# Performance work log

Hardware: AMD Instinct MI355X
Metric: run time of the kernel (lower is better)

Reference implementation:

```python
import jax, jax.numpy as jnp
import numpy as np

B = 65536
H = 32  # LSTM hidden size


def _ln(x, g, b, n_axes):
    # torch LayerNorm over the last n_axes dims, eps=1e-5, biased variance
    axes = tuple(range(x.ndim - n_axes, x.ndim))
    m = jnp.mean(x, axes, keepdims=True)
    v = jnp.var(x, axes, keepdims=True)
    return (x - m) * jax.lax.rsqrt(v + 1e-5) * g + b


def _lstm_layer(xs, Wih, Whh, bih, bhh):
    # xs: [T, B, in] ; gate order i,f,g,o as in torch
    Bn = xs.shape[1]
    h0 = jnp.zeros((Bn, H), xs.dtype)
    c0 = jnp.zeros((Bn, H), xs.dtype)
    bias = bih + bhh
    def step(carry, xt):
        h, c = carry
        gates = xt @ Wih.T + h @ Whh.T + bias
        i, f, g, o = jnp.split(gates, 4, axis=-1)
        c = jax.nn.sigmoid(f) * c + jax.nn.sigmoid(i) * jnp.tanh(g)
        h = jax.nn.sigmoid(o) * jnp.tanh(c)
        return (h, c), h
    _, hs = jax.lax.scan(step, (h0, c0), xs)
    return hs  # [T, B, H]


def _conv(x, W, b, pad_w):
    y = jax.lax.conv_general_dilated(
        x, W, (1, 1), [(0, 0), (pad_w, pad_w)],
        dimension_numbers=('NCHW', 'OIHW', 'NCHW'))
    return y + b[None, :, None, None]


def _forward(x,
             lstm_Wih0, lstm_Whh0, lstm_bih0, lstm_bhh0,
             lstm_Wih1, lstm_Whh1, lstm_bih1, lstm_bhh1,
             lstm_fcW, lstm_fcb,
             cv2_W, cv2_b, cv2_g, cv2_beta,
             cv3_W, cv3_b, cv3_g, cv3_beta,
             f1_W, f1_b, f1_g, f1_beta,
             f2_W, f2_b, f2_g, f2_beta,
             f3_W, f3_b, f3_g, f3_beta):
    Bn = x.shape[0]
    # the nested torch.cat loops are exactly this reshape: [B,12] -> [B,4,3]
    pos = x[:, 0, 1, 104:116].reshape(Bn, 4, 3)
    pos_r = pos[:, 3, :]                       # [B,3]
    # 2-layer LSTM, last-step output -> fc (run under no_grad in original)
    h1 = _lstm_layer(jnp.swapaxes(pos, 0, 1), lstm_Wih0, lstm_Whh0, lstm_bih0, lstm_bhh0)
    h2 = _lstm_layer(h1, lstm_Wih1, lstm_Whh1, lstm_bih1, lstm_bhh1)
    pos_p = h2[-1] @ lstm_fcW.T + lstm_fcb     # [B,3]
    pos_p = jax.lax.stop_gradient(pos_p)       # torch.no_grad in predict()
    vel = (pos_p - pos_r) / 0.1                # [B,3]
    # CSI conv branch
    csi = x[:, :, :, 1:103]                    # [B,1,3,102]
    out2 = jax.nn.relu(_ln(_conv(csi, cv2_W, cv2_b, 2), cv2_g, cv2_beta, 3))   # [B,4,1,102]
    out3 = jax.nn.relu(_ln(_conv(out2, cv3_W, cv3_b, 0), cv3_g, cv3_beta, 3))  # [B,1,1,102]
    out4 = jnp.concatenate([out3[:, 0, 0, :], pos_p, vel], axis=-1)            # [B,108]
    h = jax.nn.relu(_ln(out4 @ f1_W.T + f1_b, f1_g, f1_beta, 1))
    h = jax.nn.relu(_ln(h @ f2_W.T + f2_b, f2_g, f2_beta, 1))
    out = jax.nn.sigmoid(_ln(h @ f3_W.T + f3_b, f3_g, f3_beta, 1))             # [B,102]
    return out


def setup_inputs() -> dict:
    key = jax.random.key(0)
    ks = iter(jax.random.split(key, 64))
    def rn(shape, s=0.05):
        return jax.random.normal(next(ks), shape, jnp.float32) * s
    return dict(
        x=jax.random.normal(next(ks), (B, 1, 3, 116), jnp.float32),
        lstm_Wih0=rn((4 * H, 3)), lstm_Whh0=rn((4 * H, H)),
        lstm_bih0=rn((4 * H,)), lstm_bhh0=rn((4 * H,)),
        lstm_Wih1=rn((4 * H, H)), lstm_Whh1=rn((4 * H, H)),
        lstm_bih1=rn((4 * H,)), lstm_bhh1=rn((4 * H,)),
        lstm_fcW=rn((3, H)), lstm_fcb=rn((3,)),
        cv2_W=rn((4, 1, 3, 5)), cv2_b=rn((4,)),
        cv2_g=jnp.ones((4, 1, 102)), cv2_beta=jnp.zeros((4, 1, 102)),
        cv3_W=rn((1, 4, 1, 1)), cv3_b=rn((1,)),
        cv3_g=jnp.ones((1, 1, 102)), cv3_beta=jnp.zeros((1, 1, 102)),
        f1_W=rn((32, 108)), f1_b=rn((32,)),
        f1_g=jnp.ones((32,)), f1_beta=jnp.zeros((32,)),
        f2_W=rn((32, 32)), f2_b=rn((32,)),
        f2_g=jnp.ones((32,)), f2_beta=jnp.zeros((32,)),
        f3_W=rn((102, 32)), f3_b=rn((102,)),
        f3_g=jnp.ones((102,)), f3_beta=jnp.zeros((102,)),
    )


def reference(x,
              lstm_Wih0, lstm_Whh0, lstm_bih0, lstm_bhh0,
              lstm_Wih1, lstm_Whh1, lstm_bih1, lstm_bhh1,
              lstm_fcW, lstm_fcb,
              cv2_W, cv2_b, cv2_g, cv2_beta,
              cv3_W, cv3_b, cv3_g, cv3_beta,
              f1_W, f1_b, f1_g, f1_beta,
              f2_W, f2_b, f2_g, f2_beta,
              f3_W, f3_b, f3_g, f3_beta):
    return _forward(x,
                    lstm_Wih0, lstm_Whh0, lstm_bih0, lstm_bhh0,
                    lstm_Wih1, lstm_Whh1, lstm_bih1, lstm_bhh1,
                    lstm_fcW, lstm_fcb,
                    cv2_W, cv2_b, cv2_g, cv2_beta,
                    cv3_W, cv3_b, cv3_g, cv3_beta,
                    f1_W, f1_b, f1_g, f1_beta,
                    f2_W, f2_b, f2_g, f2_beta,
                    f3_W, f3_b, f3_g, f3_beta)
```

## Files before the change

kernel.cpp:

```cpp
#include <hip/hip_runtime.h>

#define DI __device__ __forceinline__
#define NSAMP 65536

typedef __attribute__((ext_vector_type(4))) float f32x4;
typedef __attribute__((ext_vector_type(8))) short short8;
typedef __attribute__((ext_vector_type(4))) short short4v;

DI float frcp(float x){ return __builtin_amdgcn_rcpf(x); }
DI float frsq(float x){ return __builtin_amdgcn_rsqf(x); }
DI float sigmf(float x){ return frcp(1.f + __expf(-x)); }
DI float tanhf_(float x){ return 1.f - 2.f*frcp(__expf(2.f*x) + 1.f); }
DI unsigned short f2bf(float f){
  unsigned u = __float_as_uint(f);
  return (unsigned short)((u + 0x7FFFu + ((u>>16)&1u)) >> 16);
}
DI float bf2f(unsigned short h){ return __uint_as_float(((unsigned)h)<<16); }

struct Params {
  const float* __restrict__ x;
  const float* __restrict__ pv;
  const float* __restrict__ ptail;
  const unsigned short* __restrict__ frags;
  const float* __restrict__ Wih0; const float* __restrict__ Whh0;
  const float* __restrict__ bih0; const float* __restrict__ bhh0;
  const float* __restrict__ Wih1; const float* __restrict__ Whh1;
  const float* __restrict__ bih1; const float* __restrict__ bhh1;
  const float* __restrict__ fcW;  const float* __restrict__ fcb;
  const float* __restrict__ W2;   const float* __restrict__ b2;
  const float* __restrict__ g2;   const float* __restrict__ be2;
  const float* __restrict__ W3;   const float* __restrict__ b3;
  const float* __restrict__ g3;   const float* __restrict__ be3;
  const float* __restrict__ W1f;  const float* __restrict__ b1f;
  const float* __restrict__ g1f;  const float* __restrict__ be1f;
  const float* __restrict__ W2f;  const float* __restrict__ b2f;
  const float* __restrict__ g2f;  const float* __restrict__ be2f;
  const float* __restrict__ W3f;  const float* __restrict__ b3f;
  const float* __restrict__ g3f;  const float* __restrict__ be3f;
  float* __restrict__ out;
};

#define PT_G2   0
#define PT_BE2  408
#define PT_G3   816
#define PT_BE3  918
#define PT_B1F  1020
#define PT_G1F  1052
#define PT_BE1F 1084
#define PT_B2F  1116
#define PT_G2F  1148
#define PT_BE2F 1180
#define PT_B3F  1212
#define PT_G3F  1314
#define PT_BE3F 1416
#define PT_N    1518
#define NFRAG   49

__global__ __launch_bounds__(256,1) void prep_kernel(Params p,
    unsigned short* __restrict__ frags, float* __restrict__ bsum,
    float* __restrict__ ptail){
  const int tid = threadIdx.x;
  if(tid < 64){
    const int l15 = tid & 15, g4 = tid >> 4;
    const float* mats[3] = {p.Whh0, p.Wih1, p.Whh1};
    for(int m=0;m<3;m++)
      for(int t=0;t<8;t++){
        const int n = 16*t + l15;
        unsigned short* dst = &frags[((size_t)(m*8+t)*64 + tid)*8];
        for(int j=0;j<4;j++){
          dst[j]   = f2bf(mats[m][n*32 + 4*g4 + j]);
          dst[4+j] = f2bf(mats[m][n*32 + 16 + 4*g4 + j]);
        }
      }
    for(int t=0;t<8;t++){
      const int n = 16*t + l15;
      unsigned short* dst = &frags[((size_t)(24+t)*64 + tid)*8];
      for(int j=0;j<4;j++){
        int k = 4*g4 + j;
        dst[j]   = (k < 3) ? f2bf(p.Wih0[n*3 + k]) : (unsigned short)0;
        dst[4+j] = 0;
      }
    }
    for(int kc=0;kc<4;kc++)
      for(int nt=0;nt<2;nt++){
        const int n = nt*16 + l15;
        unsigned short* dst = &frags[((size_t)(32+kc*2+nt)*64 + tid)*8];
        for(int j=0;j<4;j++){
          int k0 = kc*32 + 4*g4 + j;
          int k1 = kc*32 + 16 + 4*g4 + j;
          dst[j]   = (k0<108) ? f2bf(p.W1f[n*108+k0]) : (unsigned short)0;
          dst[4+j] = (k1<108) ? f2bf(p.W1f[n*108+k1]) : (unsigned short)0;
        }
      }
    for(int nt=0;nt<2;nt++){
      const int n = nt*16 + l15;
      unsigned short* dst = &frags[((size_t)(40+nt)*64 + tid)*8];
      for(int j=0;j<4;j++){
        dst[j]   = f2bf(p.W2f[n*32 + 4*g4 + j]);
        dst[4+j] = f2bf(p.W2f[n*32 + 16 + 4*g4 + j]);
      }
    }
    for(int nt=0;nt<7;nt++){
      const int n2 = nt*16 + l15;
      unsigned short* dst = &frags[((size_t)(42+nt)*64 + tid)*8];
      for(int j=0;j<4;j++){
        int k0 = 4*g4 + j, k1 = 16 + 4*g4 + j;
        dst[j]   = (n2<102) ? f2bf(p.W3f[n2*32+k0]) : (unsigned short)0;
        dst[4+j] = (n2<102) ? f2bf(p.W3f[n2*32+k1]) : (unsigned short)0;
      }
    }
  } else if(tid < 192){
    int i = tid - 64;
    bsum[i]       = p.bih0[i] + p.bhh0[i];
    bsum[128 + i] = p.bih1[i] + p.bhh1[i];
  }
  for(int i=tid;i<408;i+=256){ ptail[PT_G2+i]=p.g2[i]; ptail[PT_BE2+i]=p.be2[i]; }
  for(int i=tid;i<102;i+=256){
    ptail[PT_G3+i]=p.g3[i];   ptail[PT_BE3+i]=p.be3[i];
    ptail[PT_B3F+i]=p.b3f[i]; ptail[PT_G3F+i]=p.g3f[i]; ptail[PT_BE3F+i]=p.be3f[i];
  }
  if(tid<32){
    ptail[PT_B1F+tid]=p.b1f[tid];   ptail[PT_G1F+tid]=p.g1f[tid];
    ptail[PT_BE1F+tid]=p.be1f[tid]; ptail[PT_B2F+tid]=p.b2f[tid];
    ptail[PT_G2F+tid]=p.g2f[tid];   ptail[PT_BE2F+tid]=p.be2f[tid];
  }
}

DI short8 mk_afrag(const float* hbase, int l15, int g4){
  const float4* p0 = (const float4*)(hbase + l15*36 + 4*g4);
  const float4* p1 = (const float4*)(hbase + l15*36 + 16 + 4*g4);
  float4 lo = *p0; float4 hi = *p1;
  short8 s;
  s[0]=(short)f2bf(lo.x); s[1]=(short)f2bf(lo.y); s[2]=(short)f2bf(lo.z); s[3]=(short)f2bf(lo.w);
  s[4]=(short)f2bf(hi.x); s[5]=(short)f2bf(hi.y); s[6]=(short)f2bf(hi.z); s[7]=(short)f2bf(hi.w);
  return s;
}
DI short8 mk_af16(const unsigned short* lb, int off){
  short4v lo = *(const short4v*)(lb + off);
  short4v hi = *(const short4v*)(lb + off + 16);
  short8 s;
  s[0]=lo[0]; s[1]=lo[1]; s[2]=lo[2]; s[3]=lo[3];
  s[4]=hi[0]; s[5]=hi[1]; s[6]=hi[2]; s[7]=hi[3];
  return s;
}
DI short8 mk_af16_lo(const unsigned short* lb, int off){
  short4v lo = *(const short4v*)(lb + off);
  short8 s;
  s[0]=lo[0]; s[1]=lo[1]; s[2]=lo[2]; s[3]=lo[3];
  s[4]=0; s[5]=0; s[6]=0; s[7]=0;
  return s;
}

__global__ __launch_bounds__(256,1) void lstm_kernel(
    const float* __restrict__ x, const unsigned short* __restrict__ frags,
    const float* __restrict__ bsum, const float* __restrict__ fcW,
    const float* __restrict__ fcb, float* __restrict__ pv){
  __shared__ float hb[4][2][16][36];
  const int tid = threadIdx.x;
  const int w = tid >> 6, l = tid & 63;
  const int l15 = l & 15, g4 = l >> 4;
  const int base = blockIdx.x*64 + w*16;
  const float* __restrict__ xrow = x + (size_t)(base + l15)*348;

  short8 wf[4][8];
  const short8* fsrc = (const short8*)frags;
  #pragma unroll
  for(int m=0;m<4;m++)
    #pragma unroll
    for(int t=0;t<8;t++) wf[m][t] = fsrc[(m*8+t)*64 + l];

  float bfr[2][8];
  #pragma unroll
  for(int t=0;t<8;t++){
    bfr[0][t] = bsum[16*t + l15];
    bfr[1][t] = bsum[128 + 16*t + l15];
  }
  #pragma unroll
  for(int half=0; half<2; half++)
    #pragma unroll
    for(int r=0;r<4;r++){
      hb[w][0][g4*4+r][l15+16*half] = 0.f;
      hb[w][1][g4*4+r][l15+16*half] = 0.f;
    }
  float c0[8], c1[8];
  #pragma unroll
  for(int i=0;i<8;i++){ c0[i]=0.f; c1[i]=0.f; }

  #pragma unroll 1
  for(int t=0;t<4;t++){
    short8 ax;
    {
      float xv0 = xrow[220 + t*3 + 0];
      float xv1 = xrow[220 + t*3 + 1];
      float xv2 = xrow[220 + t*3 + 2];
      bool gz = (g4 == 0);
      ax[0] = gz ? (short)f2bf(xv0) : (short)0;
      ax[1] = gz ? (short)f2bf(xv1) : (short)0;
      ax[2] = gz ? (short)f2bf(xv2) : (short)0;
      ax[3]=0; ax[4]=0; ax[5]=0; ax[6]=0; ax[7]=0;
    }
    short8 ah0 = mk_afrag(&hb[w][0][0][0], l15, g4);
    f32x4 acc0[8];
    #pragma unroll
    for(int n=0;n<8;n++){
      f32x4 a; a[0]=bfr[0][n]; a[1]=bfr[0][n]; a[2]=bfr[0][n]; a[3]=bfr[0][n];
      a = __builtin_amdgcn_mfma_f32_16x16x32_bf16(ax,  wf[3][n], a, 0,0,0);
      a = __builtin_amdgcn_mfma_f32_16x16x32_bf16(ah0, wf[0][n], a, 0,0,0);
      acc0[n] = a;
    }
    #pragma unroll
    for(int half=0; half<2; half++)
      #pragma unroll
      for(int r=0;r<4;r++){
        float gi = acc0[0+half][r], gf = acc0[2+half][r];
        float gg = acc0[4+half][r], go = acc0[6+half][r];
        float cc = sigmf(gf)*c0[half*4+r] + sigmf(gi)*tanhf_(gg);
        c0[half*4+r] = cc;
        hb[w][0][g4*4+r][l15+16*half] = sigmf(go)*tanhf_(cc);
      }
    short8 ah0n = mk_afrag(&hb[w][0][0][0], l15, g4);
    short8 ah1  = mk_afrag(&hb[w][1][0][0], l15, g4);
    f32x4 acc1[8];
    #pragma unroll
    for(int n=0;n<8;n++){
      f32x4 a; a[0]=bfr[1][n]; a[1]=bfr[1][n]; a[2]=bfr[1][n]; a[3]=bfr[1][n];
      a = __builtin_amdgcn_mfma_f32_16x16x32_bf16(ah0n, wf[1][n], a, 0,0,0);
      a = __builtin_amdgcn_mfma_f32_16x16x32_bf16(ah1,  wf[2][n], a, 0,0,0);
      acc1[n] = a;
    }
    #pragma unroll
    for(int half=0; half<2; half++)
      #pragma unroll
      for(int r=0;r<4;r++){
        float gi = acc1[0+half][r], gf = acc1[2+half][r];
        float gg = acc1[4+half][r], go = acc1[6+half][r];
        float cc = sigmf(gf)*c1[half*4+r] + sigmf(gi)*tanhf_(gg);
        c1[half*4+r] = cc;
        hb[w][1][g4*4+r][l15+16*half] = sigmf(go)*tanhf_(cc);
      }
  }
  if(l < 16){
    const int gs = base + l;
    const float* xr2 = x + (size_t)gs*348;
    #pragma unroll
    for(int d=0;d<3;d++){
      float a = fcb[d];
      #pragma unroll
      for(int u=0;u<32;u++) a += hb[w][1][l][u]*fcW[d*32+u];
      float pr = xr2[229 + d];
      pv[(size_t)d*NSAMP + gs]     = a;
      pv[(size_t)(3+d)*NSAMP + gs] = (a - pr)*10.f;
    }
  }
}

DI float rg4(float v){
  v += __shfl_xor(v, 16);
  v += __shfl_xor(v, 32);
  return v;
}

__global__ __launch_bounds__(256,1) void tail_kernel(Params p){
  __shared__ float prm[PT_N];
  __shared__ unsigned int xs32[64*175];
  const int tid = threadIdx.x;
  const int w = tid >> 6, l = tid & 63;
  const int l15 = l & 15, g4 = l >> 4;
  const int base = blockIdx.x*64 + w*16;
  const int sl   = w*16 + l15;
  unsigned short* lb = (unsigned short*)(xs32 + w*16*175);
  const short8* fsrc = (const short8*)p.frags;
  const unsigned short* xsp = (const unsigned short*)xs32;

  for(int i=tid;i<PT_N;i+=256) prm[i]=p.ptail[i];
  {
    const float4* src = reinterpret_cast<const float4*>(p.x + (size_t)blockIdx.x*64*348);
    #pragma unroll 1
    for(int i=tid; i<64*87; i+=256){
      float4 v = src[i];
      int smp = i/87; int off = i - smp*87;
      unsigned lo = (unsigned)f2bf(v.x) | ((unsigned)f2bf(v.y)<<16);
      unsigned hi = (unsigned)f2bf(v.z) | ((unsigned)f2bf(v.w)<<16);
      xs32[smp*175 + off*2]     = lo;
      xs32[smp*175 + off*2 + 1] = hi;
    }
  }
  __syncthreads();

  #define LDX(r,c) bf2f(xsp[sl*350 + (r)*116 + 1 + (c)])

  const int C0   = g4*26;
  const int ncol = (g4==3) ? 24 : 26;

  unsigned o2p[52];
  float s1=0.f, s2=0.f;
  {
    float u0[3],u1[3],u2[3],u3[3],u4[3];
    #pragma unroll
    for(int r=0;r<3;r++){
      u0[r] = (C0-2 >= 0) ? LDX(r, C0-2) : 0.f;
      u1[r] = (C0-1 >= 0) ? LDX(r, C0-1) : 0.f;
      u2[r] = LDX(r, C0);
      u3[r] = LDX(r, C0+1);
      u4[r] = LDX(r, C0+2);
    }
    #pragma unroll
    for(int i=0;i<26;i++){
      float msk = (i < ncol) ? 1.f : 0.f;
      float sv[4];
      #pragma unroll
      for(int o=0;o<4;o++){
        float s = p.b2[o];
        #pragma unroll
        for(int r=0;r<3;r++)
          s += u0[r]*p.W2[o*15+r*5+0]+u1[r]*p.W2[o*15+r*5+1]+u2[r]*p.W2[o*15+r*5+2]
             + u3[r]*p.W2[o*15+r*5+3]+u4[r]*p.W2[o*15+r*5+4];
        sv[o] = s;
        s1 += msk*s; s2 += msk*s*s;
      }
      o2p[2*i]   = (unsigned)f2bf(sv[0]) | ((unsigned)f2bf(sv[1])<<16);
      o2p[2*i+1] = (unsigned)f2bf(sv[2]) | ((unsigned)f2bf(sv[3])<<16);
      int pn = C0 + i + 3;
      int pc = (pn <= 101) ? pn : 101;
      #pragma unroll
      for(int r=0;r<3;r++){
        float nv = LDX(r, pc);
        nv = (pn <= 101) ? nv : 0.f;
        u0[r]=u1[r]; u1[r]=u2[r]; u2[r]=u3[r]; u3[r]=u4[r]; u4[r]=nv;
      }
    }
  }
  #undef LDX
  float m2  = rg4(s1)*(1.f/408.f);
  float va2 = rg4(s2)*(1.f/408.f) - m2*m2;
  float rs2 = frsq(va2 + 1e-5f);

  float o3r[26];
  float s31=0.f, s32=0.f;
  {
    float b3v = p.b3[0];
    float w3v[4];
    #pragma unroll
    for(int o=0;o<4;o++) w3v[o] = p.W3[o];
    #pragma unroll
    for(int i=0;i<26;i++){
      const int wc = (C0+i <= 101) ? C0+i : 101;
      float msk = (i < ncol) ? 1.f : 0.f;
      float sv[4];
      sv[0] = bf2f((unsigned short)(o2p[2*i]    & 0xffffu));
      sv[1] = bf2f((unsigned short)(o2p[2*i]   >> 16));
      sv[2] = bf2f((unsigned short)(o2p[2*i+1]  & 0xffffu));
      sv[3] = bf2f((unsigned short)(o2p[2*i+1] >> 16));
      float o3 = b3v;
      #pragma unroll
      for(int o=0;o<4;o++){
        float nv = (sv[o] - m2)*rs2*prm[PT_G2+o*102+wc] + prm[PT_BE2+o*102+wc];
        o3 += fmaxf(nv, 0.f)*w3v[o];
      }
      s31 += msk*o3; s32 += msk*o3*o3;
      o3r[i] = o3;
    }
  }
  float m3  = rg4(s31)*(1.f/102.f);
  float va3 = rg4(s32)*(1.f/102.f) - m3*m3;
  float rs3 = frsq(va3 + 1e-5f);

  #pragma unroll
  for(int i=0;i<26;i++){
    if(i < ncol){
      const int wc = C0 + i;
      float v = fmaxf((o3r[i]-m3)*rs3*prm[PT_G3+wc] + prm[PT_BE3+wc], 0.f);
      lb[l15*116 + wc] = f2bf(v);
    }
  }
  if(l < 16){
    #pragma unroll
    for(int d=0;d<3;d++){
      lb[l*116+102+d] = f2bf(p.pv[(size_t)d*NSAMP + base + l]);
      lb[l*116+105+d] = f2bf(p.pv[(size_t)(3+d)*NSAMP + base + l]);
    }
    #pragma unroll
    for(int k=108;k<116;k++) lb[l*116+k] = 0;
  }

  f32x4 a1acc[2];
  {
    float b0v = prm[PT_B1F + l15], b1v = prm[PT_B1F + 16 + l15];
    a1acc[0] = f32x4{b0v,b0v,b0v,b0v};
    a1acc[1] = f32x4{b1v,b1v,b1v,b1v};
  }
  #pragma unroll
  for(int kc=0;kc<4;kc++){
    short8 af = (kc<3) ? mk_af16(lb, l15*116 + kc*32 + 4*g4)
                       : mk_af16_lo(lb, l15*116 + 96 + 4*g4);
    #pragma unroll
    for(int nt=0;nt<2;nt++){
      short8 bf = fsrc[(32+kc*2+nt)*64 + l];
      a1acc[nt] = __builtin_amdgcn_mfma_f32_16x16x32_bf16(af, bf, a1acc[nt], 0,0,0);
    }
  }
  {
    float m1[4], rs1[4];
    #pragma unroll
    for(int r=0;r<4;r++){
      float sm = a1acc[0][r] + a1acc[1][r];
      float sq = a1acc[0][r]*a1acc[0][r] + a1acc[1][r]*a1acc[1][r];
      #pragma unroll
      for(int st=1;st<16;st<<=1){ sm += __shfl_xor(sm,st); sq += __shfl_xor(sq,st); }
      float m = sm*(1.f/32.f);
      m1[r]=m; rs1[r]=frsq(sq*(1.f/32.f)-m*m+1e-5f);
    }
    #pragma unroll
    for(int nt=0;nt<2;nt++){
      float g  = prm[PT_G1F + nt*16 + l15];
      float be = prm[PT_BE1F + nt*16 + l15];
      #pragma unroll
      for(int r=0;r<4;r++){
        float vv = fmaxf((a1acc[nt][r]-m1[r])*rs1[r]*g + be, 0.f);
        lb[(4*g4+r)*116 + nt*16 + l15] = f2bf(vv);
      }
    }
  }

  {
    f32x4 a2acc[2];
    float b0v = prm[PT_B2F + l15], b1v = prm[PT_B2F + 16 + l15];
    a2acc[0] = f32x4{b0v,b0v,b0v,b0v};
    a2acc[1] = f32x4{b1v,b1v,b1v,b1v};
    short8 af = mk_af16(lb, l15*116 + 4*g4);
    #pragma unroll
    for(int nt=0;nt<2;nt++){
      short8 bf = fsrc[(40+nt)*64 + l];
      a2acc[nt] = __builtin_amdgcn_mfma_f32_16x16x32_bf16(af, bf, a2acc[nt], 0,0,0);
    }
    float m1[4], rs1[4];
    #pragma unroll
    for(int r=0;r<4;r++){
      float sm = a2acc[0][r] + a2acc[1][r];
      float sq = a2acc[0][r]*a2acc[0][r] + a2acc[1][r]*a2acc[1][r];
      #pragma unroll
      for(int st=1;st<16;st<<=1){ sm += __shfl_xor(sm,st); sq += __shfl_xor(sq,st); }
      float m = sm*(1.f/32.f);
      m1[r]=m; rs1[r]=frsq(sq*(1.f/32.f)-m*m+1e-5f);
    }
    #pragma unroll
    for(int nt=0;nt<2;nt++){
      float g  = prm[PT_G2F + nt*16 + l15];
      float be = prm[PT_BE2F + nt*16 + l15];
      #pragma unroll
      for(int r=0;r<4;r++){
        float vv = fmaxf((a2acc[nt][r]-m1[r])*rs1[r]*g + be, 0.f);
        lb[(4*g4+r)*116 + nt*16 + l15] = f2bf(vv);
      }
    }
  }

  {
    f32x4 a3[7];
    float mskt[7];
    #pragma unroll
    for(int nt=0;nt<7;nt++){
      int n2 = nt*16 + l15;
      mskt[nt] = (n2 < 102) ? 1.f : 0.f;
      float bv = prm[PT_B3F + ((n2<102)?n2:0)] * mskt[nt];
      a3[nt] = f32x4{bv,bv,bv,bv};
    }
    short8 af = mk_af16(lb, l15*116 + 4*g4);
    #pragma unroll
    for(int nt=0;nt<7;nt++){
      short8 bf = fsrc[(42+nt)*64 + l];
      a3[nt] = __builtin_amdgcn_mfma_f32_16x16x32_bf16(af, bf, a3[nt], 0,0,0);
    }
    float mf[4], rsf[4];
    #pragma unroll
    for(int r=0;r<4;r++){
      float sm=0.f, sq=0.f;
      #pragma unroll
      for(int nt=0;nt<7;nt++){
        float vv = a3[nt][r];
        sm += mskt[nt]*vv; sq += mskt[nt]*vv*vv;
      }
      #pragma unroll
      for(int st=1;st<16;st<<=1){ sm += __shfl_xor(sm,st); sq += __shfl_xor(sq,st); }
      float m = sm*(1.f/102.f);
      mf[r]=m; rsf[r]=frsq(sq*(1.f/102.f)-m*m+1e-5f);
    }
    #pragma unroll
    for(int nt=0;nt<7;nt++){
      int n2 = nt*16 + l15;
      if(n2 < 102){
        float g  = prm[PT_G3F + n2];
        float be = prm[PT_BE3F + n2];
        #pragma unroll
        for(int r=0;r<4;r++){
          float val = sigmf((a3[nt][r]-mf[r])*rsf[r]*g + be);
          p.out[(size_t)(base + 4*g4 + r)*102 + n2] = val;
        }
      }
    }
  }
}

template<int IN>
DI void lstm_step(const float* __restrict__ Wih, const float* __restrict__ Whh,
                  const float* __restrict__ bih, const float* __restrict__ bhh,
                  const float* xin, const float* hin, float* c, float* hout){
  #pragma unroll
  for(int j=0;j<32;j++){
    float ai = bih[j]    + bhh[j];
    float af = bih[32+j] + bhh[32+j];
    float ag = bih[64+j] + bhh[64+j];
    float ao = bih[96+j] + bhh[96+j];
    #pragma unroll
    for(int k=0;k<IN;k++){
      float xv = xin[k];
      ai += xv*Wih[j*IN+k]; af += xv*Wih[(32+j)*IN+k];
      ag += xv*Wih[(64+j)*IN+k]; ao += xv*Wih[(96+j)*IN+k];
    }
    #pragma unroll
    for(int k=0;k<32;k++){
      float hv = hin[k];
      ai += hv*Whh[j*32+k]; af += hv*Whh[(32+j)*32+k];
      ag += hv*Whh[(64+j)*32+k]; ao += hv*Whh[(96+j)*32+k];
    }
    float cc = sigmf(af)*c[j] + sigmf(ai)*tanhf_(ag);
    c[j] = cc;
    hout[j] = sigmf(ao)*tanhf_(cc);
  }
}

__global__ __launch_bounds__(128,1) void csnet_mono(Params p){
  const int tid = threadIdx.x;
  const int b = blockIdx.x*128 + tid;
  const float* __restrict__ xr = p.x + (size_t)b*348;
  __shared__ float sbuf[128*103];
  float* my = &sbuf[tid*103];
  float h0[32], c0[32], h1[32], c1[32];
  #pragma unroll
  for(int j=0;j<32;j++){ h0[j]=0.f; c0[j]=0.f; h1[j]=0.f; c1[j]=0.f; }
  #pragma unroll 1
  for(int t=0;t<4;t++){
    float xt[3];
    #pragma unroll
    for(int d=0;d<3;d++) xt[d] = xr[220 + t*3 + d];
    float hA[32], hB[32];
    lstm_step<3 >(p.Wih0,p.Whh0,p.bih0,p.bhh0, xt, h0, c0, hA);
    lstm_step<32>(p.Wih1,p.Whh1,p.bih1,p.bhh1, hA, h1, c1, hB);
    #pragma unroll
    for(int j=0;j<32;j++){ h0[j]=hA[j]; h1[j]=hB[j]; }
  }
  float pp[3], vel[3];
  #pragma unroll
  for(int d=0;d<3;d++){
    float a = p.fcb[d];
    #pragma unroll
    for(int j=0;j<32;j++) a += h1[j]*p.fcW[d*32+j];
    pp[d]  = a;
    vel[d] = (a - xr[229+d])*10.f;
  }
  float s1 = 0.f, s2 = 0.f;
  for(int w=0; w<102; ++w){
    #pragma unroll
    for(int o=0;o<4;o++){
      float s = p.b2[o];
      #pragma unroll
      for(int r=0;r<3;r++)
        #pragma unroll
        for(int kk=0;kk<5;kk++){
          int c = w - 2 + kk;
          float v = (c>=0 && c<=101) ? xr[r*116 + 1 + (c<0?0:(c>101?101:c))] : 0.f;
          s += v*p.W2[o*15 + r*5 + kk];
        }
      s1 += s; s2 += s*s;
    }
  }
  float m2  = s1*(1.f/408.f);
  float rs2 = frsq(s2*(1.f/408.f) - m2*m2 + 1e-5f);
  float s31=0.f, s32=0.f;
  for(int w=0; w<102; ++w){
    float o3 = p.b3[0];
    #pragma unroll
    for(int o=0;o<4;o++){
      float s = p.b2[o];
      #pragma unroll
      for(int r=0;r<3;r++)
        #pragma unroll
        for(int kk=0;kk<5;kk++){
          int c = w - 2 + kk;
          float v = (c>=0 && c<=101) ? xr[r*116 + 1 + (c<0?0:(c>101?101:c))] : 0.f;
          s += v*p.W2[o*15 + r*5 + kk];
        }
      float nv = (s - m2)*rs2*p.g2[o*102+w] + p.be2[o*102+w];
      o3 += fmaxf(nv, 0.f)*p.W3[o];
    }
    s31 += o3; s32 += o3*o3;
    my[w] = o3;
  }
  float m3  = s31*(1.f/102.f);
  float rs3 = frsq(s32*(1.f/102.f) - m3*m3 + 1e-5f);
  float a1[32];
  #pragma unroll
  for(int j=0;j<32;j++) a1[j] = p.b1f[j];
  for(int w=0; w<102; ++w){
    float v = fmaxf((my[w]-m3)*rs3*p.g3[w] + p.be3[w], 0.f);
    #pragma unroll
    for(int j=0;j<32;j++) a1[j] += v*p.W1f[j*108+w];
  }
  #pragma unroll
  for(int d=0;d<3;d++)
    #pragma unroll
    for(int j=0;j<32;j++){
      a1[j] += pp[d]*p.W1f[j*108+102+d];
      a1[j] += vel[d]*p.W1f[j*108+105+d];
    }
  {
    float s=0.f,qq=0.f;
    #pragma unroll
    for(int j=0;j<32;j++){ s+=a1[j]; qq+=a1[j]*a1[j]; }
    float m=s*(1.f/32.f), rs=frsq(qq*(1.f/32.f)-m*m+1e-5f);
    #pragma unroll
    for(int j=0;j<32;j++) a1[j]=fmaxf((a1[j]-m)*rs*p.g1f[j]+p.be1f[j],0.f);
  }
  float a2[32];
  #pragma unroll
  for(int j=0;j<32;j++){
    float a = p.b2f[j];
    #pragma unroll
    for(int k=0;k<32;k++) a += a1[k]*p.W2f[j*32+k];
    a2[j]=a;
  }
  {
    float s=0.f,qq=0.f;
    #pragma unroll
    for(int j=0;j<32;j++){ s+=a2[j]; qq+=a2[j]*a2[j]; }
    float m=s*(1.f/32.f), rs=frsq(qq*(1.f/32.f)-m*m+1e-5f);
    #pragma unroll
    for(int j=0;j<32;j++) a2[j]=fmaxf((a2[j]-m)*rs*p.g2f[j]+p.be2f[j],0.f);
  }
  float t1=0.f,t2=0.f;
  for(int w=0;w<102;++w){
    float a = p.b3f[w];
    #pragma unroll
    for(int j=0;j<32;j++) a += a2[j]*p.W3f[w*32+j];
    t1+=a; t2+=a*a;
    my[w]=a;
  }
  float mf=t1*(1.f/102.f), rsf=frsq(t2*(1.f/102.f)-mf*mf+1e-5f);
  for(int w=0;w<102;++w) my[w]=sigmf((my[w]-mf)*rsf*p.g3f[w]+p.be3f[w]);
  __syncthreads();
  float* op = p.out + (size_t)blockIdx.x*13056;
  #pragma unroll 1
  for(int m=0;m<26;m++){
    int i4 = tid + 128*m;
    if(i4 < 3264){
      int i0=i4*4;
      float4 v;
      #pragma unroll
      for(int ee=0;ee<4;ee++){
        int idx=i0+ee; int sm=idx/102; int wd=idx-sm*102;
        ((float*)&v)[ee]=sbuf[sm*103+wd];
      }
      *reinterpret_cast<float4*>(op+i0)=v;
    }
  }
}

extern "C" void kernel_launch(void* const* d_in, const int* in_sizes, int n_in,
                              void* d_out, int out_size, void* d_ws, size_t ws_size,
                              hipStream_t stream) {
  (void)in_sizes; (void)n_in; (void)out_size;
  Params p;
  p.x    = (const float*)d_in[0];
  p.Wih0 = (const float*)d_in[1];  p.Whh0 = (const float*)d_in[2];
  p.bih0 = (const float*)d_in[3];  p.bhh0 = (const float*)d_in[4];
  p.Wih1 = (const float*)d_in[5];  p.Whh1 = (const float*)d_in[6];
  p.bih1 = (const float*)d_in[7];  p.bhh1 = (const float*)d_in[8];
  p.fcW  = (const float*)d_in[9];  p.fcb  = (const float*)d_in[10];
  p.W2   = (const float*)d_in[11]; p.b2   = (const float*)d_in[12];
  p.g2   = (const float*)d_in[13]; p.be2  = (const float*)d_in[14];
  p.W3   = (const float*)d_in[15]; p.b3   = (const float*)d_in[16];
  p.g3   = (const float*)d_in[17]; p.be3  = (const float*)d_in[18];
  p.W1f  = (const float*)d_in[19]; p.b1f  = (const float*)d_in[20];
  p.g1f  = (const float*)d_in[21]; p.be1f = (const float*)d_in[22];
  p.W2f  = (const float*)d_in[23]; p.b2f  = (const float*)d_in[24];
  p.g2f  = (const float*)d_in[25]; p.be2f = (const float*)d_in[26];
  p.W3f  = (const float*)d_in[27]; p.b3f  = (const float*)d_in[28];
  p.g3f  = (const float*)d_in[29]; p.be3f = (const float*)d_in[30];
  p.out  = (float*)d_out;

  const size_t PV_F   = (size_t)6*NSAMP;
  const size_t BS_F   = 256;
  const size_t FRAG_BYTES = (size_t)NFRAG*64*8*2;
  const size_t head_f = PV_F + BS_F + PT_N;
  const size_t need = head_f*4 + FRAG_BYTES;

  if(ws_size >= need){
    float* pv    = (float*)d_ws;
    float* bsum  = pv + PV_F;
    float* ptail = bsum + BS_F;
    unsigned short* frags = (unsigned short*)(ptail + PT_N);
    p.pv = pv; p.ptail = ptail; p.frags = frags;
    prep_kernel<<<1, 256, 0, stream>>>(p, frags, bsum, ptail);
    lstm_kernel<<<NSAMP/64, 256, 0, stream>>>(p.x, frags, bsum, p.fcW, p.fcb, pv);
    tail_kernel<<<NSAMP/64, 256, 0, stream>>>(p);
  } else {
    p.pv = nullptr; p.ptail = nullptr; p.frags = nullptr;
    csnet_mono<<<NSAMP/128, 128, 0, stream>>>(p);
  }
}
```

Baseline: 118.6 us.

## Fuse LSTM kernel into tail kernel, keeping LSTM outputs in registers

Merges the separate LSTM kernel into the tail kernel. The LSTM hidden state now lives in the shared-memory staging buffer that is later reused for x, and the predicted position and velocity stay in registers instead of going through a global workspace round-trip. LSTM weight fragments are read from global per MFMA instead of being held in registers. This removes one kernel launch and the global writes and reads of the intermediate, at the cost of serialising the LSTM ahead of the CSI branch inside each block and adding an extra barrier.

```diff
diff --git a/kernel.cpp b/kernel.cpp
--- a/kernel.cpp
+++ b/kernel.cpp
@@ -19,8 +19,8 @@
 
 struct Params {
   const float* __restrict__ x;
-  const float* __restrict__ pv;
   const float* __restrict__ ptail;
+  const float* __restrict__ bsum;
   const unsigned short* __restrict__ frags;
   const float* __restrict__ Wih0; const float* __restrict__ Whh0;
   const float* __restrict__ bih0; const float* __restrict__ bhh0;
@@ -151,116 +151,13 @@
   return s;
 }
 
-__global__ __launch_bounds__(256,1) void lstm_kernel(
-    const float* __restrict__ x, const unsigned short* __restrict__ frags,
-    const float* __restrict__ bsum, const float* __restrict__ fcW,
-    const float* __restrict__ fcb, float* __restrict__ pv){
-  __shared__ float hb[4][2][16][36];
-  const int tid = threadIdx.x;
-  const int w = tid >> 6, l = tid & 63;
-  const int l15 = l & 15, g4 = l >> 4;
-  const int base = blockIdx.x*64 + w*16;
-  const float* __restrict__ xrow = x + (size_t)(base + l15)*348;
-
-  short8 wf[4][8];
-  const short8* fsrc = (const short8*)frags;
-  #pragma unroll
-  for(int m=0;m<4;m++)
-    #pragma unroll
-    for(int t=0;t<8;t++) wf[m][t] = fsrc[(m*8+t)*64 + l];
-
-  float bfr[2][8];
-  #pragma unroll
-  for(int t=0;t<8;t++){
-    bfr[0][t] = bsum[16*t + l15];
-    bfr[1][t] = bsum[128 + 16*t + l15];
-  }
-  #pragma unroll
-  for(int half=0; half<2; half++)
-    #pragma unroll
-    for(int r=0;r<4;r++){
-      hb[w][0][g4*4+r][l15+16*half] = 0.f;
-      hb[w][1][g4*4+r][l15+16*half] = 0.f;
-    }
-  float c0[8], c1[8];
-  #pragma unroll
-  for(int i=0;i<8;i++){ c0[i]=0.f; c1[i]=0.f; }
-
-  #pragma unroll 1
-  for(int t=0;t<4;t++){
-    short8 ax;
-    {
-      float xv0 = xrow[220 + t*3 + 0];
-      float xv1 = xrow[220 + t*3 + 1];
-      float xv2 = xrow[220 + t*3 + 2];
-      bool gz = (g4 == 0);
-      ax[0] = gz ? (short)f2bf(xv0) : (short)0;
-      ax[1] = gz ? (short)f2bf(xv1) : (short)0;
-      ax[2] = gz ? (short)f2bf(xv2) : (short)0;
-      ax[3]=0; ax[4]=0; ax[5]=0; ax[6]=0; ax[7]=0;
-    }
-    short8 ah0 = mk_afrag(&hb[w][0][0][0], l15, g4);
-    f32x4 acc0[8];
-    #pragma unroll
-    for(int n=0;n<8;n++){
-      f32x4 a; a[0]=bfr[0][n]; a[1]=bfr[0][n]; a[2]=bfr[0][n]; a[3]=bfr[0][n];
-      a = __builtin_amdgcn_mfma_f32_16x16x32_bf16(ax,  wf[3][n], a, 0,0,0);
-      a = __builtin_amdgcn_mfma_f32_16x16x32_bf16(ah0, wf[0][n], a, 0,0,0);
-      acc0[n] = a;
-    }
-    #pragma unroll
-    for(int half=0; half<2; half++)
-      #pragma unroll
-      for(int r=0;r<4;r++){
-        float gi = acc0[0+half][r], gf = acc0[2+half][r];
-        float gg = acc0[4+half][r], go = acc0[6+half][r];
-        float cc = sigmf(gf)*c0[half*4+r] + sigmf(gi)*tanhf_(gg);
-        c0[half*4+r] = cc;
-        hb[w][0][g4*4+r][l15+16*half] = sigmf(go)*tanhf_(cc);
-      }
-    short8 ah0n = mk_afrag(&hb[w][0][0][0], l15, g4);
-    short8 ah1  = mk_afrag(&hb[w][1][0][0], l15, g4);
-    f32x4 acc1[8];
-    #pragma unroll
-    for(int n=0;n<8;n++){
-      f32x4 a; a[0]=bfr[1][n]; a[1]=bfr[1][n]; a[2]=bfr[1][n]; a[3]=bfr[1][n];
-      a = __builtin_amdgcn_mfma_f32_16x16x32_bf16(ah0n, wf[1][n], a, 0,0,0);
-      a = __builtin_amdgcn_mfma_f32_16x16x32_bf16(ah1,  wf[2][n], a, 0,0,0);
-      acc1[n] = a;
-    }
-    #pragma unroll
-    for(int half=0; half<2; half++)
-      #pragma unroll
-      for(int r=0;r<4;r++){
-        float gi = acc1[0+half][r], gf = acc1[2+half][r];
-        float gg = acc1[4+half][r], go = acc1[6+half][r];
-        float cc = sigmf(gf)*c1[half*4+r] + sigmf(gi)*tanhf_(gg);
-        c1[half*4+r] = cc;
-        hb[w][1][g4*4+r][l15+16*half] = sigmf(go)*tanhf_(cc);
-      }
-  }
-  if(l < 16){
-    const int gs = base + l;
-    const float* xr2 = x + (size_t)gs*348;
-    #pragma unroll
-    for(int d=0;d<3;d++){
-      float a = fcb[d];
-      #pragma unroll
-      for(int u=0;u<32;u++) a += hb[w][1][l][u]*fcW[d*32+u];
-      float pr = xr2[229 + d];
-      pv[(size_t)d*NSAMP + gs]     = a;
-      pv[(size_t)(3+d)*NSAMP + gs] = (a - pr)*10.f;
-    }
-  }
-}
-
 DI float rg4(float v){
   v += __shfl_xor(v, 16);
   v += __shfl_xor(v, 32);
   return v;
 }
 
-__global__ __launch_bounds__(256,1) void tail_kernel(Params p){
+__global__ __launch_bounds__(256,1) void fused_kernel(Params p){
   __shared__ float prm[PT_N];
   __shared__ unsigned int xs32[64*175];
   const int tid = threadIdx.x;
@@ -271,8 +168,106 @@
   unsigned short* lb = (unsigned short*)(xs32 + w*16*175);
   const short8* fsrc = (const short8*)p.frags;
   const unsigned short* xsp = (const unsigned short*)xs32;
+  float* hbF  = (float*)xs32;
+  float* posB = (float*)(xs32 + 4800);
 
   for(int i=tid;i<PT_N;i+=256) prm[i]=p.ptail[i];
+  {
+    int smp = tid >> 2, q = tid & 3;
+    const float4* ps = (const float4*)(p.x + (size_t)(blockIdx.x*64+smp)*348 + 220 + q*4);
+    float4 v = *ps;
+    posB[smp*17 + q*4 + 0] = v.x;
+    posB[smp*17 + q*4 + 1] = v.y;
+    posB[smp*17 + q*4 + 2] = v.z;
+    posB[smp*17 + q*4 + 3] = v.w;
+  }
+  #pragma unroll
+  for(int half=0; half<2; half++)
+    #pragma unroll
+    for(int r=0;r<4;r++){
+      hbF[w*1152 +       (g4*4+r)*36 + l15+16*half] = 0.f;
+      hbF[w*1152 + 576 + (g4*4+r)*36 + l15+16*half] = 0.f;
+    }
+  __syncthreads();
+
+  float pp[3], vel[3];
+  {
+    float bfr[2][8];
+    #pragma unroll
+    for(int t=0;t<8;t++){
+      bfr[0][t] = p.bsum[16*t + l15];
+      bfr[1][t] = p.bsum[128 + 16*t + l15];
+    }
+    float c0[8], c1[8];
+    #pragma unroll
+    for(int i=0;i<8;i++){ c0[i]=0.f; c1[i]=0.f; }
+    const float* myPos = &posB[sl*17];
+
+    #pragma unroll 1
+    for(int t=0;t<4;t++){
+      short8 ax;
+      {
+        float xv0 = myPos[t*3+0], xv1 = myPos[t*3+1], xv2 = myPos[t*3+2];
+        bool gz = (g4 == 0);
+        ax[0] = gz ? (short)f2bf(xv0) : (short)0;
+        ax[1] = gz ? (short)f2bf(xv1) : (short)0;
+        ax[2] = gz ? (short)f2bf(xv2) : (short)0;
+        ax[3]=0; ax[4]=0; ax[5]=0; ax[6]=0; ax[7]=0;
+      }
+      short8 ah0 = mk_afrag(&hbF[w*1152], l15, g4);
+      f32x4 acc0[8];
+      #pragma unroll
+      for(int n=0;n<8;n++){
+        f32x4 a; a[0]=bfr[0][n]; a[1]=bfr[0][n]; a[2]=bfr[0][n]; a[3]=bfr[0][n];
+        a = __builtin_amdgcn_mfma_f32_16x16x32_bf16(ax,  fsrc[(24+n)*64 + l], a, 0,0,0);
+        a = __builtin_amdgcn_mfma_f32_16x16x32_bf16(ah0, fsrc[n*64 + l],      a, 0,0,0);
+        acc0[n] = a;
+      }
+      #pragma unroll
+      for(int half=0; half<2; half++)
+        #pragma unroll
+        for(int r=0;r<4;r++){
+          float gi = acc0[0+half][r], gf = acc0[2+half][r];
+          float gg = acc0[4+half][r], go = acc0[6+half][r];
+          float cc = sigmf(gf)*c0[half*4+r] + sigmf(gi)*tanhf_(gg);
+          c0[half*4+r] = cc;
+          hbF[w*1152 + (g4*4+r)*36 + l15+16*half] = sigmf(go)*tanhf_(cc);
+        }
+      short8 ah0n = mk_afrag(&hbF[w*1152], l15, g4);
+      short8 ah1  = mk_afrag(&hbF[w*1152 + 576], l15, g4);
+      f32x4 acc1[8];
+      #pragma unroll
+      for(int n=0;n<8;n++){
+        f32x4 a; a[0]=bfr[1][n]; a[1]=bfr[1][n]; a[2]=bfr[1][n]; a[3]=bfr[1][n];
+        a = __builtin_amdgcn_mfma_f32_16x16x32_bf16(ah0n, fsrc[(8+n)*64 + l],  a, 0,0,0);
+        a = __builtin_amdgcn_mfma_f32_16x16x32_bf16(ah1,  fsrc[(16+n)*64 + l], a, 0,0,0);
+        acc1[n] = a;
+      }
+      #pragma unroll
+      for(int half=0; half<2; half++)
+        #pragma unroll
+        for(int r=0;r<4;r++){
+          float gi = acc1[0+half][r], gf = acc1[2+half][r];
+          float gg = acc1[4+half][r], go = acc1[6+half][r];
+          float cc = sigmf(gf)*c1[half*4+r] + sigmf(gi)*tanhf_(gg);
+          c1[half*4+r] = cc;
+          hbF[w*1152 + 576 + (g4*4+r)*36 + l15+16*half] = sigmf(go)*tanhf_(cc);
+        }
+    }
+    if(l < 16){
+      const float* hrow = &hbF[w*1152 + 576 + l*36];
+      #pragma unroll
+      for(int d=0;d<3;d++){
+        float a = p.fcb[d];
+        #pragma unroll
+        for(int u=0;u<32;u++) a += hrow[u]*p.fcW[d*32+u];
+        pp[d]  = a;
+        vel[d] = (a - posB[(w*16 + l)*17 + 9 + d])*10.f;
+      }
+    }
+  }
+  __syncthreads();
+
   {
     const float4* src = reinterpret_cast<const float4*>(p.x + (size_t)blockIdx.x*64*348);
     #pragma unroll 1
@@ -288,7 +283,6 @@
   __syncthreads();
 
   #define LDX(r,c) bf2f(xsp[sl*350 + (r)*116 + 1 + (c)])
-
   const int C0   = g4*26;
   const int ncol = (g4==3) ? 24 : 26;
 
@@ -376,8 +370,8 @@
   if(l < 16){
     #pragma unroll
     for(int d=0;d<3;d++){
-      lb[l*116+102+d] = f2bf(p.pv[(size_t)d*NSAMP + base + l]);
-      lb[l*116+105+d] = f2bf(p.pv[(size_t)(3+d)*NSAMP + base + l]);
+      lb[l*116+102+d] = f2bf(pp[d]);
+      lb[l*116+105+d] = f2bf(vel[d]);
     }
     #pragma unroll
     for(int k=108;k<116;k++) lb[l*116+k] = 0;
@@ -688,23 +682,20 @@
   p.g3f  = (const float*)d_in[29]; p.be3f = (const float*)d_in[30];
   p.out  = (float*)d_out;
 
-  const size_t PV_F   = (size_t)6*NSAMP;
   const size_t BS_F   = 256;
   const size_t FRAG_BYTES = (size_t)NFRAG*64*8*2;
-  const size_t head_f = PV_F + BS_F + PT_N;
+  const size_t head_f = BS_F + PT_N;
   const size_t need = head_f*4 + FRAG_BYTES;
 
   if(ws_size >= need){
-    float* pv    = (float*)d_ws;
-    float* bsum  = pv + PV_F;
+    float* bsum  = (float*)d_ws;
     float* ptail = bsum + BS_F;
     unsigned short* frags = (unsigned short*)(ptail + PT_N);
-    p.pv = pv; p.ptail = ptail; p.frags = frags;
+    p.ptail = ptail; p.bsum = bsum; p.frags = frags;
     prep_kernel<<<1, 256, 0, stream>>>(p, frags, bsum, ptail);
-    lstm_kernel<<<NSAMP/64, 256, 0, stream>>>(p.x, frags, bsum, p.fcW, p.fcb, pv);
-    tail_kernel<<<NSAMP/64, 256, 0, stream>>>(p);
+    fused_kernel<<<NSAMP/64, 256, 0, stream>>>(p);
   } else {
-    p.pv = nullptr; p.ptail = nullptr; p.frags = nullptr;
+    p.ptail = nullptr; p.bsum = nullptr; p.frags = nullptr;
     csnet_mono<<<NSAMP/128, 128, 0, stream>>>(p);
   }
 }
```

Result: slower. 141.0 us (+18.9%).
